# Kernel tuning notes

Hardware: AMD Instinct MI355X
Metric: run time of the kernel (lower is better)

The kernel has to match this reference:

```python
import jax, jax.numpy as jnp
import numpy as np

TEMPERATURE = 2.5  # TopKRouter temperature from MoELayer.__init__
TOPK = 2


def setup_inputs() -> dict:
    key = jax.random.key(0)
    ks = jax.random.split(key, 4)
    B, T, D, F, E = 8, 8192, 512, 2048, 8
    x = jax.random.normal(ks[0], (B, T, D), jnp.float32)
    Wr = jax.random.normal(ks[1], (D, E), jnp.float32) * (D ** -0.5)
    W1 = jax.random.normal(ks[2], (E, D, F), jnp.float32) * (D ** -0.5)
    b1 = jnp.zeros((E, F), jnp.float32)
    W2 = jax.random.normal(ks[3], (E, F, D), jnp.float32) * (F ** -0.5)
    b2 = jnp.zeros((E, D), jnp.float32)
    return {"x": x, "Wr": Wr, "W1": W1, "b1": b1, "W2": W2, "b2": b2}


def reference(x, Wr, W1, b1, W2, b2):
    # x: (B, T, D); eval-mode MoE: no router noise, no capacity, no dropout.
    B, T, D = x.shape
    E = Wr.shape[1]
    N = B * T
    xf = x.reshape(N, D)

    # Router: softmax(logits / temperature), then top-k, renormalize kept probs.
    logits = xf @ Wr                                  # (N, E)
    probs = jax.nn.softmax(logits / TEMPERATURE, axis=-1)
    topk_vals, topk_idx = jax.lax.top_k(probs, TOPK)  # (N, K)
    topk_vals = topk_vals / jnp.sum(topk_vals, axis=-1, keepdims=True)

    # Scatter top-k weights into per-expert combine weights w: (N, E).
    w = jnp.zeros((N, E), xf.dtype)
    w = w.at[jnp.arange(N)[:, None], topk_idx].add(topk_vals)

    # Weighted combine of expert FFN outputs (fixed small loop over E experts).
    out = jnp.zeros_like(xf)
    for e in range(E):
        h = jax.nn.gelu(xf @ W1[e] + b1[e])           # (N, F)
        out = out + w[:, e:e + 1] * (h @ W2[e] + b2[e])
    return out.reshape(B, T, D)
```

## Files before the change

kernel.cpp:

```cpp
#include <hip/hip_runtime.h>
#include <cstdint>
#include <cstddef>

#define N_TOK 65536
#define DIM 512
#define FF 2048
#define NE 8
#define HCAP 24576
#define MAXT 1536

typedef __attribute__((ext_vector_type(8))) short short8;
typedef __attribute__((ext_vector_type(4))) float f32x4;

__device__ __forceinline__ unsigned f2bf(float f) {
  unsigned u = __builtin_bit_cast(unsigned, f);
  u = u + 0x7fffu + ((u >> 16) & 1u);
  return (u >> 16) & 0xffffu;
}

__device__ __forceinline__ void gload_lds16(const void* g, void* l) {
  __builtin_amdgcn_global_load_lds((const __attribute__((address_space(1))) void*)g,
                                   (__attribute__((address_space(3))) void*)l, 16, 0, 0);
}

__global__ __launch_bounds__(256) void k_transpose_cast(
    const float* __restrict__ in, unsigned short* __restrict__ outp, int rows, int cols)
{
  __shared__ float tile[32][33];
  const float* ine = in + (size_t)blockIdx.z * rows * cols;
  unsigned short* oute = outp + (size_t)blockIdx.z * rows * cols;
  int tx = threadIdx.x & 31, ty = threadIdx.x >> 5;
  int r0 = blockIdx.y * 32, c0 = blockIdx.x * 32;
#pragma unroll
  for (int i = 0; i < 4; ++i)
    tile[ty + i*8][tx] = ine[(size_t)(r0 + ty + i*8)*cols + c0 + tx];
  __syncthreads();
#pragma unroll
  for (int i = 0; i < 4; ++i) {
    int r = c0 + ty + i*8, c = r0 + tx;
    oute[(size_t)r*rows + c] = (unsigned short)f2bf(tile[tx][ty + i*8]);
  }
}

__global__ __launch_bounds__(256) void k_router(
    const float* __restrict__ x, const float* __restrict__ Wr,
    int2* __restrict__ tinfo, int* __restrict__ cnt)
{
  __shared__ int lcnt[8];
  int tid = threadIdx.x, lane = tid & 63, wv = tid >> 6;
  if (tid < 8) lcnt[tid] = 0;
  float wr[8][8];
#pragma unroll
  for (int j = 0; j < 8; ++j) {
    const float4* p = (const float4*)(Wr + (size_t)(lane*8 + j)*NE);
    float4 a = p[0], b = p[1];
    wr[j][0]=a.x; wr[j][1]=a.y; wr[j][2]=a.z; wr[j][3]=a.w;
    wr[j][4]=b.x; wr[j][5]=b.y; wr[j][6]=b.z; wr[j][7]=b.w;
  }
  __syncthreads();
  int t0 = blockIdx.x*64 + wv*16;
  for (int it = 0; it < 16; ++it) {
    int t = t0 + it;
    const float4* xp = (const float4*)(x + (size_t)t*DIM + lane*8);
    float4 v0 = xp[0], v1 = xp[1];
    float xv[8] = {v0.x,v0.y,v0.z,v0.w,v1.x,v1.y,v1.z,v1.w};
    float lg[8];
#pragma unroll
    for (int e2 = 0; e2 < 8; ++e2) lg[e2] = 0.f;
#pragma unroll
    for (int j = 0; j < 8; ++j)
#pragma unroll
      for (int e2 = 0; e2 < 8; ++e2) lg[e2] += xv[j]*wr[j][e2];
#pragma unroll
    for (int off = 32; off >= 1; off >>= 1)
#pragma unroll
      for (int e2 = 0; e2 < 8; ++e2) lg[e2] += __shfl_xor(lg[e2], off, 64);
    int e0 = 0; float v0m = lg[0];
#pragma unroll
    for (int e2 = 1; e2 < 8; ++e2) if (lg[e2] > v0m) { v0m = lg[e2]; e0 = e2; }
    int e1 = -1; float v1m = -3.0e38f;
#pragma unroll
    for (int e2 = 0; e2 < 8; ++e2) if (e2 != e0 && lg[e2] > v1m) { v1m = lg[e2]; e1 = e2; }
    float w0 = 1.f / (1.f + __expf((v1m - v0m) * 0.4f));
    if (lane == 0) {
      atomicAdd(&lcnt[e0], 1);
      atomicAdd(&lcnt[e1], 1);
      tinfo[t] = make_int2(e0 | (e1 << 8), __float_as_int(w0));
    }
  }
  __syncthreads();
  if (tid < 8) atomicAdd(&cnt[tid*16], lcnt[tid]);
}

__global__ void k_offsets(int* cnt) {
  if (threadIdx.x == 0) {
    int base = 0, tb = 0;
    for (int e2 = 0; e2 < 8; ++e2) {
      int c = cnt[e2*16]; if (c > HCAP) c = HCAP;
      cnt[e2*16 + 1] = base;
      base += cnt[e2*16];
      cnt[e2*16 + 2] = 0;
      cnt[e2*16 + 3] = tb;
      tb += (c + 127) >> 7;
    }
    cnt[135] = tb;
  }
}

__global__ __launch_bounds__(256) void k_fill(
    const float* __restrict__ x, const int2* __restrict__ tinfo,
    unsigned short* __restrict__ xg, int* __restrict__ tokl,
    float* __restrict__ pwl, int* __restrict__ cnt)
{
  __shared__ int lc[8], lbase[8], gb[8];
  __shared__ unsigned char ce[128];
  __shared__ int csl[128];
  __shared__ float cw[128];
  int tid = threadIdx.x;
  if (tid < 8) { lc[tid] = 0; gb[tid] = cnt[tid*16 + 1]; }
  __syncthreads();
  if (tid < 64) {
    int t = blockIdx.x*64 + tid;
    int2 inf = tinfo[t];
    int e0 = inf.x & 0xff, e1 = (inf.x >> 8) & 0xff;
    float w0 = __int_as_float(inf.y);
    int i0 = tid*2, i1 = i0 + 1;
    ce[i0] = (unsigned char)e0; cw[i0] = w0;        csl[i0] = atomicAdd(&lc[e0], 1);
    ce[i1] = (unsigned char)e1; cw[i1] = 1.f - w0;  csl[i1] = atomicAdd(&lc[e1], 1);
  }
  __syncthreads();
  if (tid < 8) lbase[tid] = atomicAdd(&cnt[tid*16 + 2], lc[tid]);
  __syncthreads();
  int lane = tid & 63, wv = tid >> 6;
#pragma unroll
  for (int j = 0; j < 32; ++j) {
    int i = wv*32 + j;
    int t = blockIdx.x*64 + (i >> 1);
    int e2 = ce[i];
    int gpos = gb[e2] + lbase[e2] + csl[i];
    const float4* src = (const float4*)(x + (size_t)t*DIM + lane*8);
    float4 v0 = src[0], v1 = src[1];
    uint4 pk;
    pk.x = f2bf(v0.x) | (f2bf(v0.y) << 16);
    pk.y = f2bf(v0.z) | (f2bf(v0.w) << 16);
    pk.z = f2bf(v1.x) | (f2bf(v1.y) << 16);
    pk.w = f2bf(v1.z) | (f2bf(v1.w) << 16);
    *(uint4*)(xg + (size_t)gpos*DIM + lane*8) = pk;
    if (lane == 0) { tokl[gpos] = t; pwl[gpos] = cw[i]; }
  }
}

__device__ __forceinline__ void stage128(
    const unsigned short* __restrict__ src, size_t stride, int k0,
    unsigned short* __restrict__ buf, int tid)
{
#pragma unroll
  for (int j = 0; j < 4; ++j) {
    int lrow = j*32 + (tid >> 3);
    gload_lds16(src + (size_t)lrow*stride + k0 + (((tid & 7) ^ (lrow & 7)) << 3),
                buf + j*2048 + tid*8);
  }
}

__device__ __forceinline__ void gemm128(
    const unsigned short* __restrict__ Asrc, size_t Astride,
    const unsigned short* __restrict__ Bsrc, size_t Bstride,
    int nk, unsigned short* __restrict__ As, unsigned short* __restrict__ Bs,
    f32x4 acc[4][4], int tid)
{
  const int lane = tid & 63, wv = tid >> 6;
  const int r16 = lane & 15, g4 = lane >> 4;
  const int wm = wv >> 1, wn = wv & 1;

  stage128(Asrc, Astride, 0, As, tid);
  stage128(Bsrc, Bstride, 0, Bs, tid);
  __syncthreads();

  int buf = 0;
  for (int kk = 0; kk < nk; ++kk) {
    if (kk + 1 < nk) {
      stage128(Asrc, Astride, (kk + 1)*64, As + (buf ^ 1)*8192, tid);
      stage128(Bsrc, Bstride, (kk + 1)*64, Bs + (buf ^ 1)*8192, tid);
    }
    const unsigned short* ab = As + buf*8192;
    const unsigned short* bb = Bs + buf*8192;
    short8 af[4][2], bf[4][2];
#pragma unroll
    for (int mf = 0; mf < 4; ++mf) {
      int row = wm*64 + mf*16 + r16;
#pragma unroll
      for (int k2 = 0; k2 < 2; ++k2)
        af[mf][k2] = *(const short8*)(ab + row*64 + ((((k2 << 2) + g4) ^ (row & 7)) << 3));
    }
#pragma unroll
    for (int nf = 0; nf < 4; ++nf) {
      int row = wn*64 + nf*16 + r16;
#pragma unroll
      for (int k2 = 0; k2 < 2; ++k2)
        bf[nf][k2] = *(const short8*)(bb + row*64 + ((((k2 << 2) + g4) ^ (row & 7)) << 3));
    }
    __builtin_amdgcn_s_setprio(1);
#pragma unroll
    for (int k2 = 0; k2 < 2; ++k2)
#pragma unroll
      for (int mf = 0; mf < 4; ++mf)
#pragma unroll
        for (int nf = 0; nf < 4; ++nf)
          acc[mf][nf] = __builtin_amdgcn_mfma_f32_16x16x32_bf16(
              af[mf][k2], bf[nf][k2], acc[mf][nf], 0, 0, 0);
    __builtin_amdgcn_s_setprio(0);
    __syncthreads();
    buf ^= 1;
  }
}

__device__ __forceinline__ int tile_expert(const int* cnt, int gt) {
  int e = 0;
#pragma unroll
  for (int k = 1; k < 8; ++k) if (gt >= cnt[k*16 + 3]) e = k;
  return e;
}

__global__ __launch_bounds__(256, 2) void k_gemm1(
    const unsigned short* __restrict__ xg, const unsigned short* __restrict__ w1t,
    const float* __restrict__ b1, const int* __restrict__ cnt,
    unsigned short* __restrict__ h, int T0, int cap)
{
  const int bid = blockIdx.x;
  const int lt = (bid >> 7)*8 + (bid & 7);
  const int n  = (bid >> 3) & 15;
  const int gt = T0 + lt;
  if (lt >= cap || gt >= cnt[135]) return;
  const int e = tile_expert(cnt, gt);
  const int m = gt - cnt[e*16 + 3];
  const int count0 = cnt[e*16];
  const int count = count0 < HCAP ? count0 : HCAP;
  const int row0 = m*128;
  const int gbase = cnt[e*16 + 1];

  __shared__ __align__(16) unsigned short lds[32768];
  unsigned short* As = lds;
  unsigned short* Bs = lds + 16384;

  const int tid = threadIdx.x, lane = tid & 63, wv = tid >> 6;
  const int r16 = lane & 15, g4 = lane >> 4;
  const int wm = wv >> 1, wn = wv & 1;

  const f32x4 fz = {0.f, 0.f, 0.f, 0.f};
  f32x4 acc[4][4];
#pragma unroll
  for (int a = 0; a < 4; ++a)
#pragma unroll
    for (int b = 0; b < 4; ++b) acc[a][b] = fz;

  gemm128(xg + (size_t)(gbase + row0)*DIM, DIM,
          w1t + (size_t)e*FF*DIM + (size_t)(n*128)*DIM, DIM,
          DIM/64, As, Bs, acc, tid);

  float b1v[4];
#pragma unroll
  for (int nf = 0; nf < 4; ++nf)
    b1v[nf] = b1[(size_t)e*FF + n*128 + wn*64 + nf*16 + r16];

  unsigned short* hs = lds;
#pragma unroll
  for (int mf = 0; mf < 4; ++mf)
#pragma unroll
    for (int nf = 0; nf < 4; ++nf) {
      int col = wn*64 + nf*16 + r16;
#pragma unroll
      for (int i = 0; i < 4; ++i) {
        int row = wm*64 + mf*16 + g4*4 + i;
        float v = acc[mf][nf][i] + b1v[nf];
        float u = 0.7978845608028654f * (v + 0.044715f*v*v*v);
        float gl = v / (1.f + __expf(-2.f*u));
        hs[row*136 + col] = (unsigned short)f2bf(gl);
      }
    }
  __syncthreads();
  unsigned short* hdst = h + (size_t)lt*(128*FF);
#pragma unroll
  for (int j = 0; j < 8; ++j) {
    int o = j*256 + tid;
    int row = o >> 4, part = o & 15;
    if (row0 + row < count)
      *(uint4*)(hdst + (size_t)row*FF + n*128 + part*8) =
          *(const uint4*)(hs + row*136 + part*8);
  }
}

__global__ __launch_bounds__(256, 2) void k_gemm2(
    const unsigned short* __restrict__ h, const unsigned short* __restrict__ w2t,
    const float* __restrict__ b2, const int* __restrict__ tokl,
    const float* __restrict__ pwl, const int* __restrict__ cnt,
    float* __restrict__ out, int T0, int cap)
{
  const int bid = blockIdx.x;
  const int lt = (bid >> 5)*8 + (bid & 7);
  const int n  = (bid >> 3) & 3;
  const int gt = T0 + lt;
  if (lt >= cap || gt >= cnt[135]) return;
  const int e = tile_expert(cnt, gt);
  const int m = gt - cnt[e*16 + 3];
  const int count0 = cnt[e*16];
  const int count = count0 < HCAP ? count0 : HCAP;
  const int row0 = m*128;
  const int gbase = cnt[e*16 + 1];

  __shared__ __align__(16) unsigned short lds[32768];
  unsigned short* As = lds;
  unsigned short* Bs = lds + 16384;

  const int tid = threadIdx.x, lane = tid & 63, wv = tid >> 6;
  const int r16 = lane & 15, g4 = lane >> 4;
  const int wm = wv >> 1, wn = wv & 1;

  const f32x4 fz = {0.f, 0.f, 0.f, 0.f};
  f32x4 acc[4][4];
#pragma unroll
  for (int a = 0; a < 4; ++a)
#pragma unroll
    for (int b = 0; b < 4; ++b) acc[a][b] = fz;

  gemm128(h + (size_t)lt*(128*FF), FF,
          w2t + (size_t)e*DIM*FF + (size_t)(n*128)*FF, FF,
          FF/64, As, Bs, acc, tid);

  float b2v[4];
#pragma unroll
  for (int nf = 0; nf < 4; ++nf)
    b2v[nf] = b2[(size_t)e*DIM + n*128 + wn*64 + nf*16 + r16];

#pragma unroll
  for (int mf = 0; mf < 4; ++mf)
#pragma unroll
    for (int i = 0; i < 4; ++i) {
      int lrow = row0 + wm*64 + mf*16 + g4*4 + i;
      if (lrow < count) {
        int tk = tokl[gbase + lrow];
        float wg = pwl[gbase + lrow];
#pragma unroll
        for (int nf = 0; nf < 4; ++nf) {
          int d = n*128 + wn*64 + nf*16 + r16;
          atomicAdd(out + (size_t)tk*DIM + d, (acc[mf][nf][i] + b2v[nf]) * wg);
        }
      }
    }
}

extern "C" void kernel_launch(void* const* d_in, const int* in_sizes, int n_in,
                              void* d_out, int out_size, void* d_ws, size_t ws_size,
                              hipStream_t stream)
{
  const float* x  = (const float*)d_in[0];
  const float* Wr = (const float*)d_in[1];
  const float* W1 = (const float*)d_in[2];
  const float* b1 = (const float*)d_in[3];
  const float* W2 = (const float*)d_in[4];
  const float* b2 = (const float*)d_in[5];
  float* out = (float*)d_out;
  (void)in_sizes; (void)n_in;

  char* ws = (char*)d_ws;
  unsigned short* xg  = (unsigned short*)(ws);
  unsigned short* w1t = (unsigned short*)(ws + 134217728);
  unsigned short* w2t = (unsigned short*)(ws + 150994944);
  int2*  tinfo = (int2*)(ws + 167772160);
  int*   tokl  = (int*)(ws + 168296448);
  float* pwl   = (float*)(ws + 168820736);
  int*   cnt   = (int*)(ws + 169345024);
  unsigned short* h = (unsigned short*)(ws + 169346048);

  const size_t FIXED = 169346048ULL;
  const size_t TILEB = (size_t)128 * FF * 2;
  long cap_l = (ws_size > FIXED) ? (long)((ws_size - FIXED) / TILEB) : 0;
  int cap = (int)(cap_l < MAXT ? cap_l : MAXT);
  if (cap > 256) cap = 256;
  if (cap < 8)  cap = 8;
  const int nch = (MAXT + cap - 1) / cap;
  const int ngrp = (cap + 7) / 8;

  hipMemsetAsync(cnt, 0, 256*sizeof(int), stream);
  hipMemsetAsync(d_out, 0, (size_t)out_size*sizeof(float), stream);

  dim3 g1(FF/32, DIM/32, NE);
  k_transpose_cast<<<g1, 256, 0, stream>>>(W1, w1t, DIM, FF);
  dim3 g2(DIM/32, FF/32, NE);
  k_transpose_cast<<<g2, 256, 0, stream>>>(W2, w2t, FF, DIM);

  k_router<<<N_TOK/64, 256, 0, stream>>>(x, Wr, tinfo, cnt);
  k_offsets<<<1, 64, 0, stream>>>(cnt);
  k_fill<<<N_TOK/64, 256, 0, stream>>>(x, tinfo, xg, tokl, pwl, cnt);

  for (int c = 0; c < nch; ++c) {
    const int T0 = c * cap;
    k_gemm1<<<ngrp*128, 256, 0, stream>>>(xg, w1t, b1, cnt, h, T0, cap);
    k_gemm2<<<ngrp*32,  256, 0, stream>>>(h, w2t, b2, tokl, pwl, cnt, out, T0, cap);
  }
}
```

Baseline: 1.224 ms.

## Gather token rows directly in GEMM1 instead of materializing expert-sorted copies

The router kernel now writes a bf16 copy of x once per token, and the fill kernel only writes token indices and weights instead of copying each token twice into an expert-sorted buffer. GEMM1 then gathers A rows through the token index list when loading into LDS. This removes the extra scatter-copy traffic and frees workspace, which allows larger h chunks. GEMM1's tile-to-block mapping is also reordered so the 16 N-tiles of one M-tile are adjacent, which should improve reuse of the gathered rows. The cost is indirect, non-contiguous row loads in GEMM1.

```diff
diff --git a/kernel.cpp b/kernel.cpp
--- a/kernel.cpp
+++ b/kernel.cpp
@@ -7,7 +7,7 @@
 #define FF 2048
 #define NE 8
 #define HCAP 24576
-#define MAXT 1536
+#define MAXT 1032
 
 typedef __attribute__((ext_vector_type(8))) short short8;
 typedef __attribute__((ext_vector_type(4))) float f32x4;
@@ -44,7 +44,7 @@
 
 __global__ __launch_bounds__(256) void k_router(
     const float* __restrict__ x, const float* __restrict__ Wr,
-    int2* __restrict__ tinfo, int* __restrict__ cnt)
+    unsigned short* __restrict__ xb, int2* __restrict__ tinfo, int* __restrict__ cnt)
 {
   __shared__ int lcnt[8];
   int tid = threadIdx.x, lane = tid & 63, wv = tid >> 6;
@@ -64,6 +64,12 @@
     const float4* xp = (const float4*)(x + (size_t)t*DIM + lane*8);
     float4 v0 = xp[0], v1 = xp[1];
     float xv[8] = {v0.x,v0.y,v0.z,v0.w,v1.x,v1.y,v1.z,v1.w};
+    uint4 pk;
+    pk.x = f2bf(xv[0]) | (f2bf(xv[1]) << 16);
+    pk.y = f2bf(xv[2]) | (f2bf(xv[3]) << 16);
+    pk.z = f2bf(xv[4]) | (f2bf(xv[5]) << 16);
+    pk.w = f2bf(xv[6]) | (f2bf(xv[7]) << 16);
+    *(uint4*)(xb + (size_t)t*DIM + lane*8) = pk;
     float lg[8];
 #pragma unroll
     for (int e2 = 0; e2 < 8; ++e2) lg[e2] = 0.f;
@@ -107,9 +113,8 @@
   }
 }
 
-__global__ __launch_bounds__(256) void k_fill(
-    const float* __restrict__ x, const int2* __restrict__ tinfo,
-    unsigned short* __restrict__ xg, int* __restrict__ tokl,
+__global__ __launch_bounds__(128) void k_fill(
+    const int2* __restrict__ tinfo, int* __restrict__ tokl,
     float* __restrict__ pwl, int* __restrict__ cnt)
 {
   __shared__ int lc[8], lbase[8], gb[8];
@@ -131,23 +136,10 @@
   __syncthreads();
   if (tid < 8) lbase[tid] = atomicAdd(&cnt[tid*16 + 2], lc[tid]);
   __syncthreads();
-  int lane = tid & 63, wv = tid >> 6;
-#pragma unroll
-  for (int j = 0; j < 32; ++j) {
-    int i = wv*32 + j;
-    int t = blockIdx.x*64 + (i >> 1);
-    int e2 = ce[i];
-    int gpos = gb[e2] + lbase[e2] + csl[i];
-    const float4* src = (const float4*)(x + (size_t)t*DIM + lane*8);
-    float4 v0 = src[0], v1 = src[1];
-    uint4 pk;
-    pk.x = f2bf(v0.x) | (f2bf(v0.y) << 16);
-    pk.y = f2bf(v0.z) | (f2bf(v0.w) << 16);
-    pk.z = f2bf(v1.x) | (f2bf(v1.y) << 16);
-    pk.w = f2bf(v1.z) | (f2bf(v1.w) << 16);
-    *(uint4*)(xg + (size_t)gpos*DIM + lane*8) = pk;
-    if (lane == 0) { tokl[gpos] = t; pwl[gpos] = cw[i]; }
-  }
+  int e = ce[tid];
+  int p = gb[e] + lbase[e] + csl[tid];
+  tokl[p] = blockIdx.x*64 + (tid >> 1);
+  pwl[p]  = cw[tid];
 }
 
 __device__ __forceinline__ void stage128(
@@ -162,58 +154,6 @@
   }
 }
 
-__device__ __forceinline__ void gemm128(
-    const unsigned short* __restrict__ Asrc, size_t Astride,
-    const unsigned short* __restrict__ Bsrc, size_t Bstride,
-    int nk, unsigned short* __restrict__ As, unsigned short* __restrict__ Bs,
-    f32x4 acc[4][4], int tid)
-{
-  const int lane = tid & 63, wv = tid >> 6;
-  const int r16 = lane & 15, g4 = lane >> 4;
-  const int wm = wv >> 1, wn = wv & 1;
-
-  stage128(Asrc, Astride, 0, As, tid);
-  stage128(Bsrc, Bstride, 0, Bs, tid);
-  __syncthreads();
-
-  int buf = 0;
-  for (int kk = 0; kk < nk; ++kk) {
-    if (kk + 1 < nk) {
-      stage128(Asrc, Astride, (kk + 1)*64, As + (buf ^ 1)*8192, tid);
-      stage128(Bsrc, Bstride, (kk + 1)*64, Bs + (buf ^ 1)*8192, tid);
-    }
-    const unsigned short* ab = As + buf*8192;
-    const unsigned short* bb = Bs + buf*8192;
-    short8 af[4][2], bf[4][2];
-#pragma unroll
-    for (int mf = 0; mf < 4; ++mf) {
-      int row = wm*64 + mf*16 + r16;
-#pragma unroll
-      for (int k2 = 0; k2 < 2; ++k2)
-        af[mf][k2] = *(const short8*)(ab + row*64 + ((((k2 << 2) + g4) ^ (row & 7)) << 3));
-    }
-#pragma unroll
-    for (int nf = 0; nf < 4; ++nf) {
-      int row = wn*64 + nf*16 + r16;
-#pragma unroll
-      for (int k2 = 0; k2 < 2; ++k2)
-        bf[nf][k2] = *(const short8*)(bb + row*64 + ((((k2 << 2) + g4) ^ (row & 7)) << 3));
-    }
-    __builtin_amdgcn_s_setprio(1);
-#pragma unroll
-    for (int k2 = 0; k2 < 2; ++k2)
-#pragma unroll
-      for (int mf = 0; mf < 4; ++mf)
-#pragma unroll
-        for (int nf = 0; nf < 4; ++nf)
-          acc[mf][nf] = __builtin_amdgcn_mfma_f32_16x16x32_bf16(
-              af[mf][k2], bf[nf][k2], acc[mf][nf], 0, 0, 0);
-    __builtin_amdgcn_s_setprio(0);
-    __syncthreads();
-    buf ^= 1;
-  }
-}
-
 __device__ __forceinline__ int tile_expert(const int* cnt, int gt) {
   int e = 0;
 #pragma unroll
@@ -222,13 +162,13 @@
 }
 
 __global__ __launch_bounds__(256, 2) void k_gemm1(
-    const unsigned short* __restrict__ xg, const unsigned short* __restrict__ w1t,
+    const unsigned short* __restrict__ xb, const unsigned short* __restrict__ w1t,
     const float* __restrict__ b1, const int* __restrict__ cnt,
-    unsigned short* __restrict__ h, int T0, int cap)
+    const int* __restrict__ tokl, unsigned short* __restrict__ h, int T0, int cap)
 {
   const int bid = blockIdx.x;
-  const int lt = (bid >> 7)*8 + (bid & 7);
-  const int n  = (bid >> 3) & 15;
+  const int n  = (bid & 7) | (((bid >> 3) & 1) << 3);
+  const int lt = bid >> 4;
   const int gt = T0 + lt;
   if (lt >= cap || gt >= cnt[135]) return;
   const int e = tile_expert(cnt, gt);
@@ -246,6 +186,22 @@
   const int r16 = lane & 15, g4 = lane >> 4;
   const int wm = wv >> 1, wn = wv & 1;
 
+  int rows4[4];
+#pragma unroll
+  for (int j = 0; j < 4; ++j) {
+    int rr = row0 + j*32 + (tid >> 3);
+    if (rr > count - 1) rr = count - 1;
+    rows4[j] = tokl[gbase + rr];
+  }
+  const int axor = ((tid & 7) ^ ((tid >> 3) & 7)) << 3;
+  const unsigned short* w1p = w1t + (size_t)e*FF*DIM + (size_t)(n*128)*DIM;
+
+  auto stageA = [&](unsigned short* buf, int k0) {
+#pragma unroll
+    for (int j = 0; j < 4; ++j)
+      gload_lds16(xb + (size_t)rows4[j]*DIM + k0 + axor, buf + j*2048 + tid*8);
+  };
+
   const f32x4 fz = {0.f, 0.f, 0.f, 0.f};
   f32x4 acc[4][4];
 #pragma unroll
@@ -253,9 +209,45 @@
 #pragma unroll
     for (int b = 0; b < 4; ++b) acc[a][b] = fz;
 
-  gemm128(xg + (size_t)(gbase + row0)*DIM, DIM,
-          w1t + (size_t)e*FF*DIM + (size_t)(n*128)*DIM, DIM,
-          DIM/64, As, Bs, acc, tid);
+  stageA(As, 0);
+  stage128(w1p, DIM, 0, Bs, tid);
+  __syncthreads();
+  int buf = 0;
+  for (int kk = 0; kk < DIM/64; ++kk) {
+    if (kk + 1 < DIM/64) {
+      stageA(As + (buf ^ 1)*8192, (kk + 1)*64);
+      stage128(w1p, DIM, (kk + 1)*64, Bs + (buf ^ 1)*8192, tid);
+    }
+    const unsigned short* ab = As + buf*8192;
+    const unsigned short* bb = Bs + buf*8192;
+    short8 af[4][2], bf[4][2];
+#pragma unroll
+    for (int mf = 0; mf < 4; ++mf) {
+      int row = wm*64 + mf*16 + r16;
+#pragma unroll
+      for (int k2 = 0; k2 < 2; ++k2)
+        af[mf][k2] = *(const short8*)(ab + row*64 + ((((k2 << 2) + g4) ^ (row & 7)) << 3));
+    }
+#pragma unroll
+    for (int nf = 0; nf < 4; ++nf) {
+      int row = wn*64 + nf*16 + r16;
+#pragma unroll
+      for (int k2 = 0; k2 < 2; ++k2)
+        bf[nf][k2] = *(const short8*)(bb + row*64 + ((((k2 << 2) + g4) ^ (row & 7)) << 3));
+    }
+    __builtin_amdgcn_s_setprio(1);
+#pragma unroll
+    for (int k2 = 0; k2 < 2; ++k2)
+#pragma unroll
+      for (int mf = 0; mf < 4; ++mf)
+#pragma unroll
+        for (int nf = 0; nf < 4; ++nf)
+          acc[mf][nf] = __builtin_amdgcn_mfma_f32_16x16x32_bf16(
+              af[mf][k2], bf[nf][k2], acc[mf][nf], 0, 0, 0);
+    __builtin_amdgcn_s_setprio(0);
+    __syncthreads();
+    buf ^= 1;
+  }
 
   float b1v[4];
 #pragma unroll
@@ -315,6 +307,9 @@
   const int r16 = lane & 15, g4 = lane >> 4;
   const int wm = wv >> 1, wn = wv & 1;
 
+  const unsigned short* ap = h + (size_t)lt*(128*FF);
+  const unsigned short* bp = w2t + (size_t)e*DIM*FF + (size_t)(n*128)*FF;
+
   const f32x4 fz = {0.f, 0.f, 0.f, 0.f};
   f32x4 acc[4][4];
 #pragma unroll
@@ -322,9 +317,45 @@
 #pragma unroll
     for (int b = 0; b < 4; ++b) acc[a][b] = fz;
 
-  gemm128(h + (size_t)lt*(128*FF), FF,
-          w2t + (size_t)e*DIM*FF + (size_t)(n*128)*FF, FF,
-          FF/64, As, Bs, acc, tid);
+  stage128(ap, FF, 0, As, tid);
+  stage128(bp, FF, 0, Bs, tid);
+  __syncthreads();
+  int buf = 0;
+  for (int kk = 0; kk < FF/64; ++kk) {
+    if (kk + 1 < FF/64) {
+      stage128(ap, FF, (kk + 1)*64, As + (buf ^ 1)*8192, tid);
+      stage128(bp, FF, (kk + 1)*64, Bs + (buf ^ 1)*8192, tid);
+    }
+    const unsigned short* ab = As + buf*8192;
+    const unsigned short* bb = Bs + buf*8192;
+    short8 af[4][2], bf[4][2];
+#pragma unroll
+    for (int mf = 0; mf < 4; ++mf) {
+      int row = wm*64 + mf*16 + r16;
+#pragma unroll
+      for (int k2 = 0; k2 < 2; ++k2)
+        af[mf][k2] = *(const short8*)(ab + row*64 + ((((k2 << 2) + g4) ^ (row & 7)) << 3));
+    }
+#pragma unroll
+    for (int nf = 0; nf < 4; ++nf) {
+      int row = wn*64 + nf*16 + r16;
+#pragma unroll
+      for (int k2 = 0; k2 < 2; ++k2)
+        bf[nf][k2] = *(const short8*)(bb + row*64 + ((((k2 << 2) + g4) ^ (row & 7)) << 3));
+    }
+    __builtin_amdgcn_s_setprio(1);
+#pragma unroll
+    for (int k2 = 0; k2 < 2; ++k2)
+#pragma unroll
+      for (int mf = 0; mf < 4; ++mf)
+#pragma unroll
+        for (int nf = 0; nf < 4; ++nf)
+          acc[mf][nf] = __builtin_amdgcn_mfma_f32_16x16x32_bf16(
+              af[mf][k2], bf[nf][k2], acc[mf][nf], 0, 0, 0);
+    __builtin_amdgcn_s_setprio(0);
+    __syncthreads();
+    buf ^= 1;
+  }
 
   float b2v[4];
 #pragma unroll
@@ -362,16 +393,16 @@
   (void)in_sizes; (void)n_in;
 
   char* ws = (char*)d_ws;
-  unsigned short* xg  = (unsigned short*)(ws);
-  unsigned short* w1t = (unsigned short*)(ws + 134217728);
-  unsigned short* w2t = (unsigned short*)(ws + 150994944);
-  int2*  tinfo = (int2*)(ws + 167772160);
-  int*   tokl  = (int*)(ws + 168296448);
-  float* pwl   = (float*)(ws + 168820736);
-  int*   cnt   = (int*)(ws + 169345024);
-  unsigned short* h = (unsigned short*)(ws + 169346048);
-
-  const size_t FIXED = 169346048ULL;
+  unsigned short* xb  = (unsigned short*)(ws);
+  unsigned short* w1t = (unsigned short*)(ws + 67108864);
+  unsigned short* w2t = (unsigned short*)(ws + 83886080);
+  int2*  tinfo = (int2*)(ws + 100663296);
+  int*   tokl  = (int*)(ws + 101187584);
+  float* pwl   = (float*)(ws + 101711872);
+  int*   cnt   = (int*)(ws + 102236160);
+  unsigned short* h = (unsigned short*)(ws + 102237184);
+
+  const size_t FIXED = 102237184ULL;
   const size_t TILEB = (size_t)128 * FF * 2;
   long cap_l = (ws_size > FIXED) ? (long)((ws_size - FIXED) / TILEB) : 0;
   int cap = (int)(cap_l < MAXT ? cap_l : MAXT);
@@ -388,13 +419,13 @@
   dim3 g2(DIM/32, FF/32, NE);
   k_transpose_cast<<<g2, 256, 0, stream>>>(W2, w2t, FF, DIM);
 
-  k_router<<<N_TOK/64, 256, 0, stream>>>(x, Wr, tinfo, cnt);
+  k_router<<<N_TOK/64, 256, 0, stream>>>(x, Wr, xb, tinfo, cnt);
   k_offsets<<<1, 64, 0, stream>>>(cnt);
-  k_fill<<<N_TOK/64, 256, 0, stream>>>(x, tinfo, xg, tokl, pwl, cnt);
+  k_fill<<<N_TOK/64, 128, 0, stream>>>(tinfo, tokl, pwl, cnt);
 
   for (int c = 0; c < nch; ++c) {
     const int T0 = c * cap;
-    k_gemm1<<<ngrp*128, 256, 0, stream>>>(xg, w1t, b1, cnt, h, T0, cap);
+    k_gemm1<<<ngrp*128, 256, 0, stream>>>(xb, w1t, b1, cnt, tokl, h, T0, cap);
     k_gemm2<<<ngrp*32,  256, 0, stream>>>(h, w2t, b2, tokl, pwl, cnt, out, T0, cap);
   }
 }
```

After: 1.181 ms. 3.5% less time.
